# Performance work log

Measured on AMD Instinct MI355X. Metric: run time of the kernel, lower is better.

Reference implementation:

```python
import jax, jax.numpy as jnp
import numpy as np

# --- constants matching DILConfig ---
N_DIFF = 1000      # num_diffusion_steps
STEPS = 4          # inference_steps
S_MAX = 4          # max_scales
BUDGET = 0.2       # entropy_budget
G0 = 2.0           # guidance_strength
ENT_LO = 0.1       # stability_threshold_low
ENT_HI = 0.5       # stability_threshold_high
B, L, C, H = 16, 1024, 128, 512


def setup_inputs() -> dict:
    key = jax.random.key(0)
    ks = jax.random.split(key, 6)
    y_obs = jax.random.normal(ks[0], (B, L, C), dtype=jnp.float32)
    mask = (jax.random.uniform(ks[1], (B, L, C)) > 0.5).astype(jnp.float32)
    z_init = jax.random.normal(ks[2], (B, L, C), dtype=jnp.float32)
    W1 = jax.random.normal(ks[3], (C, H), dtype=jnp.float32) / np.sqrt(C)
    b1 = jnp.zeros((H,), dtype=jnp.float32)
    W2 = jax.random.normal(ks[4], (H, C), dtype=jnp.float32) / np.sqrt(H)
    b2 = jnp.zeros((C,), dtype=jnp.float32)
    tw = jax.random.normal(ks[5], (H,), dtype=jnp.float32)
    return {"y_obs": y_obs, "mask": mask, "z_init": z_init,
            "W1": W1, "b1": b1, "W2": W2, "b2": b2, "tw": tw}


def _dil_forward(y_obs, mask, z_init, W1, b1, W2, b2, tw):
    # diffusion schedule (linear betas)
    betas = jnp.linspace(1e-4, 0.02, N_DIFF, dtype=jnp.float32)
    ac = jnp.cumprod(1.0 - betas)
    alpha = jnp.sqrt(ac)                     # sqrt_alphas_cumprod
    sigma = jnp.sqrt(1.0 - ac)               # sqrt_one_minus_alphas_cumprod
    lam = jnp.log(alpha) - jnp.log(sigma)    # log-SNR/2

    step = N_DIFF // STEPS
    ks = [N_DIFF - 1 - i * step for i in range(STEPS)]

    def score(z, k):
        # epsilon predictor: channel MLP with scalar time feature
        t_feat = jnp.float32(k) / N_DIFF
        h = jax.nn.gelu(jnp.einsum('blc,ch->blh', z, W1) + b1 + t_feat * tw)
        return jnp.einsum('blh,hc->blc', h, W2) + b2

    z = z_init
    for k in ks:  # fixed small unrolled loop over inference steps
        kp = max(k - step, 0)
        eps = score(z, k)                                   # [B,L,C]
        h_lam = lam[kp] - lam[k]
        base_a = alpha[kp] / alpha[k]
        base_b = sigma[kp] * (jnp.exp(h_lam) - 1.0)

        # entropy map: batch-mean |eps| per pixel
        ent_pix = jnp.mean(jnp.abs(eps), axis=0)            # [L,C]

        # self-guidance on observed entries
        obs_err = (z - y_obs) * mask
        guidance = -obs_err / (jnp.var(obs_err) + 1e-8)     # [B,L,C]

        z_new = z
        # coarse -> fine so finer-scale selected nodes overwrite coarser ones
        for s in range(S_MAX - 1, -1, -1):
            w = 2 ** s
            pooled = ent_pix.reshape(L // w, w, C // w, w).mean(axis=(1, 3))
            Knodes = max(1, int(BUDGET * pooled.size))
            _, idx = jax.lax.top_k(pooled.ravel(), Knodes)
            selg = jnp.zeros((pooled.size,), jnp.float32).at[idx].set(1.0)
            selg = selg.reshape(pooled.shape)
            sel = jnp.repeat(jnp.repeat(selg, w, axis=0), w, axis=1)     # [L,C]
            ent_up = jnp.repeat(jnp.repeat(pooled, w, axis=0), w, axis=1)

            # adaptive solver order from entropy stability thresholds
            order = (1.0 + (ent_up > ENT_LO).astype(jnp.float32)
                         + (ent_up > ENT_HI).astype(jnp.float32))
            corr = (1.0 + (order - 1.0) * 0.5 * h_lam
                        + (order - 1.0) * (order - 2.0) / 6.0 * h_lam ** 2)
            gs = G0 * ent_up / (ent_up + 1.0)               # adaptive guidance

            cand = base_a * z - base_b * (corr * eps) + gs * guidance
            z_new = jnp.where(sel[None, :, :] > 0, cand, z_new)
        z = z_new
    return z


def reference(y_obs, mask, z_init, W1, b1, W2, b2, tw):
    return _dil_forward(y_obs, mask, z_init, W1, b1, W2, b2, tw)
```

## Files before the change

### kernel.cpp

```cpp
#include <hip/hip_runtime.h>
#include <math.h>
#include <stdint.h>

#define L_DIM 1024
#define C_DIM 128
#define H_DIM 512
#define B_DIM 16
#define LC (L_DIM * C_DIM)
#define BLC (B_DIM * LC)

typedef __attribute__((ext_vector_type(8))) short short8;
typedef __attribute__((ext_vector_type(4))) float floatx4;

__device__ __forceinline__ unsigned fordbits(unsigned u) {
    return (u & 0x80000000u) ? ~u : (u | 0x80000000u);
}

__device__ __forceinline__ void split3(float x, unsigned& uh, unsigned& um,
                                       unsigned& ul) {
    uh = __float_as_uint(x);
    const float r1 = x - __uint_as_float(uh & 0xffff0000u);
    um = __float_as_uint(r1);
    const float r2 = r1 - __uint_as_float(um & 0xffff0000u);
    ul = __float_as_uint(r2);
}

__device__ __forceinline__ float gelu_fast(float x) {
    const float g = 0.7978845608028654f * (x + 0.044715f * x * x * x);
    const float e = __expf(2.0f * g);
    const float t = 1.0f - 2.0f / (e + 1.0f);
    return 0.5f * x * (1.0f + t);
}

__global__ __launch_bounds__(256) void wsplit_kernel(
    const float* __restrict__ W1, const float* __restrict__ W2,
    unsigned short* __restrict__ W1h, unsigned short* __restrict__ W1m,
    unsigned short* __restrict__ W1l, unsigned short* __restrict__ W2h,
    unsigned short* __restrict__ W2m, unsigned short* __restrict__ W2l,
    unsigned* __restrict__ zeroblk) {
    const int t = blockIdx.x * 256 + threadIdx.x;
    if (t < 16396) zeroblk[t] = 0u;
    unsigned uh, um, ul;
    if (t < 65536) {
        const int j = t & 7, lane = (t >> 3) & 63, nt = (t >> 9) & 31,
                  kt = (t >> 14) & 3;
        const int k = kt * 32 + (lane >> 4) * 8 + j;
        const int n = nt * 16 + (lane & 15);
        split3(W1[k * 512 + n], uh, um, ul);
        W1h[t] = (unsigned short)(uh >> 16);
        W1m[t] = (unsigned short)(um >> 16);
        W1l[t] = (unsigned short)(ul >> 16);
    } else {
        const int t2 = t - 65536;
        const int j = t2 & 7, lane = (t2 >> 3) & 63, nt = (t2 >> 9) & 7,
                  kt = (t2 >> 12) & 15;
        const int k = kt * 32 + (lane >> 4) * 8 + j;
        const int n = nt * 16 + (lane & 15);
        split3(W2[k * 128 + n], uh, um, ul);
        W2h[t2] = (unsigned short)(uh >> 16);
        W2m[t2] = (unsigned short)(um >> 16);
        W2l[t2] = (unsigned short)(ul >> 16);
    }
}

#define MFMA6(AH, AM, AL, BH, BM, BL, ACC)                                    \
    ACC = __builtin_amdgcn_mfma_f32_16x16x32_bf16(AL, BH, ACC, 0, 0, 0);      \
    ACC = __builtin_amdgcn_mfma_f32_16x16x32_bf16(AM, BM, ACC, 0, 0, 0);      \
    ACC = __builtin_amdgcn_mfma_f32_16x16x32_bf16(AH, BL, ACC, 0, 0, 0);      \
    ACC = __builtin_amdgcn_mfma_f32_16x16x32_bf16(AM, BH, ACC, 0, 0, 0);      \
    ACC = __builtin_amdgcn_mfma_f32_16x16x32_bf16(AH, BM, ACC, 0, 0, 0);      \
    ACC = __builtin_amdgcn_mfma_f32_16x16x32_bf16(AH, BH, ACC, 0, 0, 0);

__device__ __forceinline__ int swz(int row, int col) {
    return row * 128 + ((((col >> 3) ^ (row & 15))) << 3) + (col & 7);
}

template <int UPD>
__global__ __launch_bounds__(1024, 8) void mlp_kernel(
    float* __restrict__ z, const float* __restrict__ zr,
    const float* __restrict__ y, const float* __restrict__ mk,
    const unsigned short* __restrict__ W1h, const unsigned short* __restrict__ W1m,
    const unsigned short* __restrict__ W1l, const unsigned short* __restrict__ W2h,
    const unsigned short* __restrict__ W2m, const unsigned short* __restrict__ W2l,
    const float* __restrict__ b1, const float* __restrict__ tw,
    const float* __restrict__ b2, float t_feat,
    float* __restrict__ eps_buf, float* __restrict__ ent,
    const float* __restrict__ cA, const float* __restrict__ cB,
    const float* __restrict__ cG, float* __restrict__ accum) {
    __shared__ unsigned short lds2[2][3][4096];
    __shared__ float red1[16], red2[16];
    const int tid = threadIdx.x;
    const int w = tid >> 6, lane = tid & 63;
    const int quad = lane >> 4, m16 = lane & 15;
    const int il_w = w >> 3, w8 = w & 7;
    const int l0 = blockIdx.x * 2;

    float s1 = 0.f, s2 = 0.f;
    {
        const int f = tid * 4;
        const int r_ = f >> 7, cb = f & 127;
        const int b = r_ & 15, il = r_ >> 4, l = l0 + il;
        const size_t g = ((size_t)b * 1024 + l) * 128 + cb;
        float4 zv = *(const float4*)(zr + g);
        const float4 yv = *(const float4*)(y + g);
        const float4 mv = *(const float4*)(mk + g);
        if (UPD) {
            const float4 ev = *(const float4*)(eps_buf + g);
            const int pix = l * 128 + cb;
            const float4 a4 = *(const float4*)(cA + pix);
            const float4 b4 = *(const float4*)(cB + pix);
            const float4 g4 = *(const float4*)(cG + pix);
            zv.x = a4.x * zv.x - b4.x * ev.x - g4.x * ((zv.x - yv.x) * mv.x);
            zv.y = a4.y * zv.y - b4.y * ev.y - g4.y * ((zv.y - yv.y) * mv.y);
            zv.z = a4.z * zv.z - b4.z * ev.z - g4.z * ((zv.z - yv.z) * mv.z);
            zv.w = a4.w * zv.w - b4.w * ev.w - g4.w * ((zv.w - yv.w) * mv.w);
            *(float4*)(z + g) = zv;
        }
        float oe;
        oe = (zv.x - yv.x) * mv.x; s1 += oe; s2 += oe * oe;
        oe = (zv.y - yv.y) * mv.y; s1 += oe; s2 += oe * oe;
        oe = (zv.z - yv.z) * mv.z; s1 += oe; s2 += oe * oe;
        oe = (zv.w - yv.w) * mv.w; s1 += oe; s2 += oe * oe;

        const int base = swz(r_, cb);
        const float xs[4] = {zv.x, zv.y, zv.z, zv.w};
        ushort4 vh, vm, vl;
        unsigned uh, um, ul;
        split3(xs[0], uh, um, ul); vh.x = uh >> 16; vm.x = um >> 16; vl.x = ul >> 16;
        split3(xs[1], uh, um, ul); vh.y = uh >> 16; vm.y = um >> 16; vl.y = ul >> 16;
        split3(xs[2], uh, um, ul); vh.z = uh >> 16; vm.z = um >> 16; vl.z = ul >> 16;
        split3(xs[3], uh, um, ul); vh.w = uh >> 16; vm.w = um >> 16; vl.w = ul >> 16;
        *(ushort4*)(&lds2[0][0][base]) = vh;
        *(ushort4*)(&lds2[0][1][base]) = vm;
        *(ushort4*)(&lds2[0][2][base]) = vl;
    }
#pragma unroll
    for (int off = 32; off; off >>= 1) {
        s1 += __shfl_down(s1, off);
        s2 += __shfl_down(s2, off);
    }
    if (lane == 0) { red1[w] = s1; red2[w] = s2; }
    __syncthreads();
    if (tid == 0) {
        float a1 = 0.f, a2 = 0.f;
#pragma unroll
        for (int i = 0; i < 16; ++i) { a1 += red1[i]; a2 += red2[i]; }
        atomicAdd(&accum[0], a1);
        atomicAdd(&accum[1], a2);
    }

    floatx4 acc1[4];
#pragma unroll
    for (int i = 0; i < 4; ++i) acc1[i] = (floatx4){0.f, 0.f, 0.f, 0.f};

#pragma unroll
    for (int kt = 0; kt < 4; ++kt) {
#pragma unroll
        for (int q2 = 0; q2 < 2; ++q2) {
            const size_t off = ((size_t)(kt * 32 + q2 * 16 + w) * 64 + lane) * 8;
            const short8 bh = *(const short8*)(W1h + off);
            const short8 bm = *(const short8*)(W1m + off);
            const short8 bl = *(const short8*)(W1l + off);
#pragma unroll
            for (int il = 0; il < 2; ++il) {
                const int fb = swz(il * 16 + m16, kt * 32 + quad * 8);
                const short8 Ah = *(const short8*)(&lds2[0][0][fb]);
                const short8 Am = *(const short8*)(&lds2[0][1][fb]);
                const short8 Al = *(const short8*)(&lds2[0][2][fb]);
                floatx4 a = acc1[q2 * 2 + il];
                MFMA6(Ah, Am, Al, bh, bm, bl, a);
                acc1[q2 * 2 + il] = a;
            }
        }
    }

    floatx4 acc2 = (floatx4){0.f, 0.f, 0.f, 0.f};

#pragma unroll
    for (int q = 0; q < 4; ++q) {
        const int bi = (q & 1) ^ 1;
        if (il_w == (q & 1)) {
            const int colg = q * 128 + w8 * 16 + m16;
            const float bb = b1[colg] + t_feat * tw[colg];
            const int kcol = w8 * 16 + m16;
#pragma unroll
            for (int il = 0; il < 2; ++il) {
#pragma unroll
                for (int r = 0; r < 4; ++r) {
                    const float x = gelu_fast(acc1[(q >> 1) * 2 + il][r] + bb);
                    unsigned uh, um, ul;
                    split3(x, uh, um, ul);
                    const int idx = swz(il * 16 + quad * 4 + r, kcol);
                    lds2[bi][0][idx] = (unsigned short)(uh >> 16);
                    lds2[bi][1][idx] = (unsigned short)(um >> 16);
                    lds2[bi][2][idx] = (unsigned short)(ul >> 16);
                }
            }
        }
        __syncthreads();

#pragma unroll
        for (int ktl = 0; ktl < 4; ++ktl) {
            const int fb = swz(il_w * 16 + m16, ktl * 32 + quad * 8);
            const short8 Ah2 = *(const short8*)(&lds2[bi][0][fb]);
            const short8 Am2 = *(const short8*)(&lds2[bi][1][fb]);
            const short8 Al2 = *(const short8*)(&lds2[bi][2][fb]);
            const size_t off =
                ((size_t)((q * 4 + ktl) * 8 + w8) * 64 + lane) * 8;
            const short8 bh = *(const short8*)(W2h + off);
            const short8 bm = *(const short8*)(W2m + off);
            const short8 bl = *(const short8*)(W2l + off);
            MFMA6(Ah2, Am2, Al2, bh, bm, bl, acc2);
        }
    }

    {
        const int col = w8 * 16 + m16;
        const float bb2 = b2[col];
        float pa = 0.f;
#pragma unroll
        for (int r = 0; r < 4; ++r) {
            const float e = acc2[r] + bb2;
            const int b = quad * 4 + r;
            eps_buf[((size_t)b * 1024 + l0 + il_w) * 128 + col] = e;
            pa += fabsf(e);
        }
        pa += __shfl_xor(pa, 16);
        pa += __shfl_xor(pa, 32);
        if (quad == 0) ent[(l0 + il_w) * 128 + col] = pa * (1.0f / 16.0f);
    }
}


__global__ __launch_bounds__(256) void pools_kernel(
    const float* __restrict__ ent, float* __restrict__ p1,
    float* __restrict__ p2, float* __restrict__ p3,
    unsigned* __restrict__ ghist) {
    __shared__ unsigned lh[8192];
    const int tid = threadIdx.x;
    const int gid = blockIdx.x * 256 + tid;
    for (int i = tid; i < 8192; i += 256) lh[i] = 0u;
    __syncthreads();

    {
        const float2 ev = *(const float2*)(ent + (size_t)gid * 2);
        const unsigned b0 = fordbits(__float_as_uint(ev.x)) >> 18;
        const unsigned b1_ = fordbits(__float_as_uint(ev.y)) >> 18;
        atomicAdd(&lh[b0 >> 1], 1u << ((b0 & 1) << 4));
        atomicAdd(&lh[b1_ >> 1], 1u << ((b1_ & 1) << 4));
    }
    if (gid < 32768) {
        const int r = gid >> 6, c = gid & 63;
        float s = 0.f;
#pragma unroll
        for (int ii = 0; ii < 2; ++ii) {
            const float2 e = *(const float2*)(ent + (((r * 2 + ii) << 7) + c * 2));
            s += e.x; s += e.y;
        }
        p1[gid] = s * 0.25f;
    }
    if (gid < 8192) {
        const int r = gid >> 5, c = gid & 31;
        float s = 0.f;
#pragma unroll
        for (int ii = 0; ii < 4; ++ii) {
            const float4 e = *(const float4*)(ent + (((r * 4 + ii) << 7) + c * 4));
            s += e.x; s += e.y; s += e.z; s += e.w;
        }
        p2[gid] = s * 0.0625f;
    }
    if (gid < 2048) {
        const int r = gid >> 4, c = gid & 15;
        float s = 0.f;
#pragma unroll
        for (int ii = 0; ii < 8; ++ii) {
            const float4 ea = *(const float4*)(ent + (((r * 8 + ii) << 7) + c * 8));
            const float4 eb = *(const float4*)(ent + (((r * 8 + ii) << 7) + c * 8 + 4));
            s += ea.x; s += ea.y; s += ea.z; s += ea.w;
            s += eb.x; s += eb.y; s += eb.z; s += eb.w;
        }
        p3[gid] = s * (1.0f / 64.0f);
    }
    __syncthreads();
    for (int i = tid; i < 8192; i += 256) {
        const unsigned v = lh[i];
        if (v & 0xFFFFu) atomicAdd(&ghist[2 * i], v & 0xFFFFu);
        if (v >> 16) atomicAdd(&ghist[2 * i + 1], v >> 16);
    }
}

#define CAND_CAP 16384

template <int NPT4, int N, unsigned K>
__device__ __forceinline__ void small_select(
    const float* __restrict__ data, unsigned* __restrict__ gout, const int t,
    const int w8, unsigned* __restrict__ histcand,
    unsigned* __restrict__ part, unsigned (*hrep)[512],
    unsigned* sh_b, unsigned* sh_krem, unsigned* sh_cnt, unsigned* sh_d,
    unsigned* sh_k2) {
    float4 xv[NPT4];
#pragma unroll
    for (int i = 0; i < NPT4; ++i) {
        const int idx4 = t + i * 1024;
        if (idx4 < (N >> 2)) xv[i] = ((const float4*)data)[idx4];
        else xv[i] = (float4){-1e30f, -1e30f, -1e30f, -1e30f};
    }
    unsigned u[NPT4 * 4];
#pragma unroll
    for (int i = 0; i < NPT4; ++i) {
        u[4 * i + 0] = fordbits(__float_as_uint(xv[i].x));
        u[4 * i + 1] = fordbits(__float_as_uint(xv[i].y));
        u[4 * i + 2] = fordbits(__float_as_uint(xv[i].z));
        u[4 * i + 3] = fordbits(__float_as_uint(xv[i].w));
    }
    if (t == 0) { *sh_b = 0u; *sh_krem = 1u; *sh_cnt = 0u; *sh_d = 0u; *sh_k2 = 1u; }
    for (int i = t; i < 16384; i += 1024) histcand[i] = 0u;
    __syncthreads();
#pragma unroll
    for (int j = 0; j < NPT4 * 4; ++j) atomicAdd(&histcand[u[j] >> 18], 1u);
    __syncthreads();
    {
        unsigned s = 0;
#pragma unroll
        for (int j = 0; j < 16; ++j) s += histcand[t * 16 + j];
        part[t] = s;
    }
    __syncthreads();
    for (int off = 1; off < 1024; off <<= 1) {
        const unsigned v = (t + off < 1024) ? part[t + off] : 0u;
        __syncthreads();
        part[t] += v;
        __syncthreads();
    }
    {
        const unsigned suf = part[t];
        const unsigned sufn = (t < 1023) ? part[t + 1] : 0u;
        if (suf >= K && sufn < K) {
            unsigned run = sufn;
            for (int b = 15; b >= 0; --b) {
                const unsigned hb = histcand[t * 16 + b];
                run += hb;
                if (run >= K) {
                    *sh_b = (unsigned)(t * 16 + b);
                    *sh_krem = K - (run - hb);
                    break;
                }
            }
        }
    }
    __syncthreads();
    const unsigned b14 = *sh_b;
    unsigned krem = *sh_krem;
    __syncthreads();
#pragma unroll
    for (int j = 0; j < NPT4 * 4; ++j)
        if ((u[j] >> 18) == b14) {
            const unsigned p = atomicAdd(sh_cnt, 1u);
            if (p < CAND_CAP) histcand[p] = u[j];
        }
    __syncthreads();
    const unsigned cnt = *sh_cnt;
    const bool inlds = (cnt <= CAND_CAP);
    for (int i = t; i < 4096; i += 1024) ((unsigned*)hrep)[i] = 0u;
    __syncthreads();
    if (inlds) {
        for (unsigned i = t; i < cnt; i += 1024)
            atomicAdd(&hrep[w8][(histcand[i] >> 9) & 511u], 1u);
    } else {
#pragma unroll
        for (int j = 0; j < NPT4 * 4; ++j)
            if ((u[j] >> 18) == b14)
                atomicAdd(&hrep[w8][(u[j] >> 9) & 511u], 1u);
    }
    __syncthreads();
    if (t < 512) {
        unsigned s = 0;
#pragma unroll
        for (int r = 0; r < 8; ++r) s += hrep[r][t];
        part[t] = s;
    }
    __syncthreads();
    for (int off = 1; off < 512; off <<= 1) {
        unsigned v = 0u;
        if (t < 512) v = (t + off < 512) ? part[t + off] : 0u;
        __syncthreads();
        if (t < 512) part[t] += v;
        __syncthreads();
    }
    if (t < 512) {
        const unsigned suf = part[t];
        const unsigned sufn = (t < 511) ? part[t + 1] : 0u;
        if (suf >= krem && sufn < krem) { *sh_d = (unsigned)t; *sh_k2 = krem - sufn; }
    }
    __syncthreads();
    const unsigned dA = *sh_d;
    krem = *sh_k2;
    __syncthreads();
    for (int i = t; i < 4096; i += 1024) ((unsigned*)hrep)[i] = 0u;
    __syncthreads();
    if (inlds) {
        for (unsigned i = t; i < cnt; i += 1024) {
            const unsigned c = histcand[i];
            if (((c >> 9) & 511u) == dA) atomicAdd(&hrep[w8][c & 511u], 1u);
        }
    } else {
#pragma unroll
        for (int j = 0; j < NPT4 * 4; ++j)
            if ((u[j] >> 18) == b14 && ((u[j] >> 9) & 511u) == dA)
                atomicAdd(&hrep[w8][u[j] & 511u], 1u);
    }
    __syncthreads();
    if (t < 512) {
        unsigned s = 0;
#pragma unroll
        for (int r = 0; r < 8; ++r) s += hrep[r][t];
        part[t] = s;
    }
    __syncthreads();
    for (int off = 1; off < 512; off <<= 1) {
        unsigned v = 0u;
        if (t < 512) v = (t + off < 512) ? part[t + off] : 0u;
        __syncthreads();
        if (t < 512) part[t] += v;
        __syncthreads();
    }
    if (t < 512) {
        const unsigned suf = part[t];
        const unsigned sufn = (t < 511) ? part[t + 1] : 0u;
        if (suf >= krem && sufn < krem)
            gout[0] = (b14 << 18) | (dA << 9) | (unsigned)t;
    }
}

__global__ __launch_bounds__(1024, 1) void thresh_kernel(
    const float* __restrict__ ent, const float* __restrict__ p1,
    const float* __restrict__ p2, const float* __restrict__ p3,
    const unsigned* __restrict__ ghist, unsigned* __restrict__ gprefix) {
    const int scale = blockIdx.x, t = threadIdx.x;
    __shared__ unsigned histcand[16384];
    __shared__ unsigned part[1024];
    __shared__ unsigned hrep[8][512];
    __shared__ unsigned sh_b, sh_krem, sh_cnt, sh_d, sh_k2;
    const int w8 = (t >> 6) & 7;

    if (scale == 1) {
        small_select<8, 32768, 6553u>(p1, &gprefix[1], t, w8, histcand, part,
                                      hrep, &sh_b, &sh_krem, &sh_cnt, &sh_d,
                                      &sh_k2);
        return;
    }
    if (scale == 2) {
        small_select<2, 8192, 1638u>(p2, &gprefix[2], t, w8, histcand, part,
                                     hrep, &sh_b, &sh_krem, &sh_cnt, &sh_d,
                                     &sh_k2);
        return;
    }
    if (scale == 3) {
        small_select<1, 2048, 409u>(p3, &gprefix[3], t, w8, histcand, part,
                                    hrep, &sh_b, &sh_krem, &sh_cnt, &sh_d,
                                    &sh_k2);
        return;
    }

    const unsigned K = 26214u;
    if (t == 0) { sh_b = 0u; sh_krem = 1u; sh_cnt = 0u; sh_d = 0u; sh_k2 = 1u; }

    {
        unsigned s = 0;
        const uint4* h4 = (const uint4*)(ghist + t * 16);
#pragma unroll
        for (int j = 0; j < 4; ++j) {
            const uint4 x = h4[j];
            s += x.x + x.y + x.z + x.w;
        }
        part[t] = s;
    }
    __syncthreads();
    for (int off = 1; off < 1024; off <<= 1) {
        const unsigned v = (t + off < 1024) ? part[t + off] : 0u;
        __syncthreads();
        part[t] += v;
        __syncthreads();
    }
    {
        const unsigned suf = part[t];
        const unsigned sufn = (t < 1023) ? part[t + 1] : 0u;
        if (suf >= K && sufn < K) {
            unsigned run = sufn;
            for (int b = 15; b >= 0; --b) {
                const unsigned hb = ghist[t * 16 + b];
                run += hb;
                if (run >= K) {
                    sh_b = (unsigned)(t * 16 + b);
                    sh_krem = K - (run - hb);
                    break;
                }
            }
        }
    }
    __syncthreads();
    const unsigned b14 = sh_b;
    unsigned krem = sh_krem;

    for (int base = 0; base < 32768; base += 8192) {
        float4 w4[8];
#pragma unroll
        for (int i = 0; i < 8; ++i)
            w4[i] = ((const float4*)ent)[base + i * 1024 + t];
#pragma unroll
        for (int i = 0; i < 8; ++i) {
            const float xs[4] = {w4[i].x, w4[i].y, w4[i].z, w4[i].w};
#pragma unroll
            for (int j = 0; j < 4; ++j) {
                const unsigned uu = fordbits(__float_as_uint(xs[j]));
                if ((uu >> 18) == b14) {
                    const unsigned p = atomicAdd(&sh_cnt, 1u);
                    if (p < CAND_CAP) histcand[p] = uu;
                }
            }
        }
    }
    __syncthreads();
    const unsigned cnt = sh_cnt;
    const bool inlds = (cnt <= CAND_CAP);

    for (int i = t; i < 4096; i += 1024) ((unsigned*)hrep)[i] = 0u;
    __syncthreads();
    if (inlds) {
        for (unsigned i = t; i < cnt; i += 1024)
            atomicAdd(&hrep[w8][(histcand[i] >> 9) & 511u], 1u);
    } else {
        for (int base = 0; base < 32768; base += 8192) {
            float4 w4[8];
#pragma unroll
            for (int i = 0; i < 8; ++i)
                w4[i] = ((const float4*)ent)[base + i * 1024 + t];
#pragma unroll
            for (int i = 0; i < 8; ++i) {
                const float xs[4] = {w4[i].x, w4[i].y, w4[i].z, w4[i].w};
#pragma unroll
                for (int j = 0; j < 4; ++j) {
                    const unsigned uu = fordbits(__float_as_uint(xs[j]));
                    if ((uu >> 18) == b14)
                        atomicAdd(&hrep[w8][(uu >> 9) & 511u], 1u);
                }
            }
        }
    }
    __syncthreads();
    if (t < 512) {
        unsigned s = 0;
#pragma unroll
        for (int r = 0; r < 8; ++r) s += hrep[r][t];
        part[t] = s;
    }
    __syncthreads();
    for (int off = 1; off < 512; off <<= 1) {
        unsigned v = 0u;
        if (t < 512) v = (t + off < 512) ? part[t + off] : 0u;
        __syncthreads();
        if (t < 512) part[t] += v;
        __syncthreads();
    }
    if (t < 512) {
        const unsigned suf = part[t];
        const unsigned sufn = (t < 511) ? part[t + 1] : 0u;
        if (suf >= krem && sufn < krem) { sh_d = (unsigned)t; sh_k2 = krem - sufn; }
    }
    __syncthreads();
    const unsigned dA = sh_d;
    krem = sh_k2;
    __syncthreads();

    for (int i = t; i < 4096; i += 1024) ((unsigned*)hrep)[i] = 0u;
    __syncthreads();
    if (inlds) {
        for (unsigned i = t; i < cnt; i += 1024) {
            const unsigned c = histcand[i];
            if (((c >> 9) & 511u) == dA) atomicAdd(&hrep[w8][c & 511u], 1u);
        }
    } else {
        for (int base = 0; base < 32768; base += 8192) {
            float4 w4[8];
#pragma unroll
            for (int i = 0; i < 8; ++i)
                w4[i] = ((const float4*)ent)[base + i * 1024 + t];
#pragma unroll
            for (int i = 0; i < 8; ++i) {
                const float xs[4] = {w4[i].x, w4[i].y, w4[i].z, w4[i].w};
#pragma unroll
                for (int j = 0; j < 4; ++j) {
                    const unsigned uu = fordbits(__float_as_uint(xs[j]));
                    if ((uu >> 18) == b14 && ((uu >> 9) & 511u) == dA)
                        atomicAdd(&hrep[w8][uu & 511u], 1u);
                }
            }
        }
    }
    __syncthreads();
    if (t < 512) {
        unsigned s = 0;
#pragma unroll
        for (int r = 0; r < 8; ++r) s += hrep[r][t];
        part[t] = s;
    }
    __syncthreads();
    for (int off = 1; off < 512; off <<= 1) {
        unsigned v = 0u;
        if (t < 512) v = (t + off < 512) ? part[t + off] : 0u;
        __syncthreads();
        if (t < 512) part[t] += v;
        __syncthreads();
    }
    if (t < 512) {
        const unsigned suf = part[t];
        const unsigned sufn = (t < 511) ? part[t + 1] : 0u;
        if (suf >= krem && sufn < krem)
            gprefix[0] = (b14 << 18) | (dA << 9) | (unsigned)t;
    }
}

__global__ __launch_bounds__(256) void coeff_kernel(
    const float* __restrict__ ent, const float* __restrict__ p1,
    const float* __restrict__ p2, const float* __restrict__ p3,
    const unsigned* __restrict__ gprefix, const float* __restrict__ accum_si,
    float* __restrict__ cA, float* __restrict__ cB, float* __restrict__ cG,
    unsigned* __restrict__ ghist, float base_a, float base_b, float h_lam) {
    const int i = blockIdx.x * 256 + threadIdx.x;
    if (i < 16384) ghist[i] = 0u;

    const unsigned t0 = gprefix[0], t1 = gprefix[1], t2 = gprefix[2],
                   t3 = gprefix[3];
    const float mean = accum_si[0] * (1.0f / (float)BLC);
    const float var = accum_si[1] * (1.0f / (float)BLC) - mean * mean;
    const float vinv = 1.0f / (var + 1e-8f);

    const int l = i >> 7, c = i & 127;
    float ent_v = 0.f;
    bool sel = false;
    const float v0 = ent[i];
    if (fordbits(__float_as_uint(v0)) >= t0) { ent_v = v0; sel = true; }
    else {
        const float v1 = p1[((l >> 1) << 6) + (c >> 1)];
        if (fordbits(__float_as_uint(v1)) >= t1) { ent_v = v1; sel = true; }
        else {
            const float v2 = p2[((l >> 2) << 5) + (c >> 2)];
            if (fordbits(__float_as_uint(v2)) >= t2) { ent_v = v2; sel = true; }
            else {
                const float v3 = p3[((l >> 3) << 4) + (c >> 3)];
                if (fordbits(__float_as_uint(v3)) >= t3) { ent_v = v3; sel = true; }
            }
        }
    }
    if (sel) {
        float corr;
        if (ent_v > 0.5f)
            corr = 1.0f + h_lam + h_lam * h_lam * (1.0f / 3.0f);
        else if (ent_v > 0.1f)
            corr = 1.0f + 0.5f * h_lam;
        else
            corr = 1.0f;
        cA[i] = base_a;
        cB[i] = base_b * corr;
        cG[i] = (2.0f * ent_v / (ent_v + 1.0f)) * vinv;
    } else {
        cA[i] = 1.0f;
        cB[i] = 0.f;
        cG[i] = 0.f;
    }
}

__global__ __launch_bounds__(256) void update_kernel(
    float* __restrict__ z, const float* __restrict__ y,
    const float* __restrict__ mk, const float* __restrict__ eps,
    const float* __restrict__ cA, const float* __restrict__ cB,
    const float* __restrict__ cG) {
    const int idx = blockIdx.x * 256 + threadIdx.x;
    const int p = idx & (LC - 1);
    const float zi = z[idx];
    z[idx] = cA[p] * zi - cB[p] * eps[idx] - cG[p] * ((zi - y[idx]) * mk[idx]);
}

extern "C" void kernel_launch(void* const* d_in, const int* in_sizes, int n_in,
                              void* d_out, int out_size, void* d_ws,
                              size_t ws_size, hipStream_t stream) {
    const float* y_obs = (const float*)d_in[0];
    const float* mask = (const float*)d_in[1];
    const float* z_init = (const float*)d_in[2];
    const float* W1 = (const float*)d_in[3];
    const float* b1 = (const float*)d_in[4];
    const float* W2 = (const float*)d_in[5];
    const float* b2 = (const float*)d_in[6];
    const float* tw = (const float*)d_in[7];
    float* z = (float*)d_out;
    float* ws = (float*)d_ws;

    float* eps = ws;
    float* ent = ws + 2097152;
    float* p1 = ws + 2228224;
    float* p2 = ws + 2260992;
    float* p3 = ws + 2269184;
    float* cA = ws + 2271232;
    float* cB = ws + 2402304;
    float* cG = ws + 2533376;
    float* accum = ws + 2664448;
    unsigned* gprefix = (unsigned*)(ws + 2664456);
    unsigned* ghist = (unsigned*)(ws + 2664460);
    unsigned short* W1h = (unsigned short*)(ws + 2680844);
    unsigned short* W1m = (unsigned short*)(ws + 2713612);
    unsigned short* W1l = (unsigned short*)(ws + 2746380);
    unsigned short* W2h = (unsigned short*)(ws + 2779148);
    unsigned short* W2m = (unsigned short*)(ws + 2811916);
    unsigned short* W2l = (unsigned short*)(ws + 2844684);

    float alpha_[1000], sigma_[1000], lam_[1000];
    {
        float ac = 1.0f;
        for (int i = 0; i < 1000; ++i) {
            const float beta = 1e-4f + (0.02f - 1e-4f) * ((float)i / 999.0f);
            ac = ac * (1.0f - beta);
            alpha_[i] = sqrtf(ac);
            sigma_[i] = sqrtf(1.0f - ac);
            lam_[i] = logf(alpha_[i]) - logf(sigma_[i]);
        }
    }
    float tf[4], hl[4], ba[4], bb[4];
    for (int si = 0; si < 4; ++si) {
        const int k = 999 - si * 250;
        const int kp = (k - 250 > 0) ? (k - 250) : 0;
        tf[si] = (float)k / 1000.0f;
        hl[si] = lam_[kp] - lam_[k];
        ba[si] = alpha_[kp] / alpha_[k];
        bb[si] = sigma_[kp] * (expf(hl[si]) - 1.0f);
    }

    wsplit_kernel<<<512, 256, 0, stream>>>(W1, W2, W1h, W1m, W1l, W2h, W2m,
                                           W2l, (unsigned*)accum);

    for (int si = 0; si < 4; ++si) {
        const float* zrd = (si <= 1) ? z_init : z;
        if (si == 0) {
            mlp_kernel<0><<<512, 1024, 0, stream>>>(
                z, zrd, y_obs, mask, W1h, W1m, W1l, W2h, W2m, W2l, b1, tw, b2,
                tf[0], eps, ent, cA, cB, cG, accum);
        } else {
            mlp_kernel<1><<<512, 1024, 0, stream>>>(
                z, zrd, y_obs, mask, W1h, W1m, W1l, W2h, W2m, W2l, b1, tw, b2,
                tf[si], eps, ent, cA, cB, cG, accum + 2 * si);
        }
        pools_kernel<<<256, 256, 0, stream>>>(ent, p1, p2, p3, ghist);
        thresh_kernel<<<4, 1024, 0, stream>>>(ent, p1, p2, p3, ghist, gprefix);
        coeff_kernel<<<512, 256, 0, stream>>>(ent, p1, p2, p3, gprefix,
                                              accum + 2 * si, cA, cB, cG,
                                              ghist, ba[si], bb[si], hl[si]);
    }
    update_kernel<<<8192, 256, 0, stream>>>(z, y_obs, mask, eps, cA, cB, cG);
}
```

Baseline: 415.9 us.

## Process four L rows per MLP block to reuse weight fragments across more tiles

Each MLP block now handles 64 rows (4 sequence positions × 16 batch) with 8 waves instead of 32 rows with 16 waves. Each wave loads a weight fragment once and applies it to 4 row tiles, halving global/L2 weight traffic per output. The double-buffered hidden LDS tile becomes a single buffer with an extra barrier per hidden chunk. Register pressure rises and the grid shrinks to 256 blocks, which reduces occupancy and latency hiding.

```diff
diff --git a/kernel.cpp b/kernel.cpp
--- a/kernel.cpp
+++ b/kernel.cpp
@@ -76,7 +76,7 @@
 }
 
 template <int UPD>
-__global__ __launch_bounds__(1024, 8) void mlp_kernel(
+__global__ __launch_bounds__(512, 2) void mlp_kernel(
     float* __restrict__ z, const float* __restrict__ zr,
     const float* __restrict__ y, const float* __restrict__ mk,
     const unsigned short* __restrict__ W1h, const unsigned short* __restrict__ W1m,
@@ -87,17 +87,18 @@
     float* __restrict__ eps_buf, float* __restrict__ ent,
     const float* __restrict__ cA, const float* __restrict__ cB,
     const float* __restrict__ cG, float* __restrict__ accum) {
-    __shared__ unsigned short lds2[2][3][4096];
-    __shared__ float red1[16], red2[16];
+    __shared__ unsigned short zA[3][8192];
+    __shared__ unsigned short hA[3][8192];
+    __shared__ float red1[8], red2[8];
     const int tid = threadIdx.x;
     const int w = tid >> 6, lane = tid & 63;
     const int quad = lane >> 4, m16 = lane & 15;
-    const int il_w = w >> 3, w8 = w & 7;
-    const int l0 = blockIdx.x * 2;
+    const int l0 = blockIdx.x * 4;
 
     float s1 = 0.f, s2 = 0.f;
-    {
-        const int f = tid * 4;
+#pragma unroll
+    for (int e = 0; e < 4; ++e) {
+        const int f = (e * 512 + tid) * 4;
         const int r_ = f >> 7, cb = f & 127;
         const int b = r_ & 15, il = r_ >> 4, l = l0 + il;
         const size_t g = ((size_t)b * 1024 + l) * 128 + cb;
@@ -130,9 +131,9 @@
         split3(xs[1], uh, um, ul); vh.y = uh >> 16; vm.y = um >> 16; vl.y = ul >> 16;
         split3(xs[2], uh, um, ul); vh.z = uh >> 16; vm.z = um >> 16; vl.z = ul >> 16;
         split3(xs[3], uh, um, ul); vh.w = uh >> 16; vm.w = um >> 16; vl.w = ul >> 16;
-        *(ushort4*)(&lds2[0][0][base]) = vh;
-        *(ushort4*)(&lds2[0][1][base]) = vm;
-        *(ushort4*)(&lds2[0][2][base]) = vl;
+        *(ushort4*)(&zA[0][base]) = vh;
+        *(ushort4*)(&zA[1][base]) = vm;
+        *(ushort4*)(&zA[2][base]) = vl;
     }
 #pragma unroll
     for (int off = 32; off; off >>= 1) {
@@ -144,56 +145,61 @@
     if (tid == 0) {
         float a1 = 0.f, a2 = 0.f;
 #pragma unroll
-        for (int i = 0; i < 16; ++i) { a1 += red1[i]; a2 += red2[i]; }
+        for (int i = 0; i < 8; ++i) { a1 += red1[i]; a2 += red2[i]; }
         atomicAdd(&accum[0], a1);
         atomicAdd(&accum[1], a2);
     }
 
-    floatx4 acc1[4];
-#pragma unroll
-    for (int i = 0; i < 4; ++i) acc1[i] = (floatx4){0.f, 0.f, 0.f, 0.f};
+    floatx4 acc1[16];
+#pragma unroll
+    for (int i = 0; i < 16; ++i) acc1[i] = (floatx4){0.f, 0.f, 0.f, 0.f};
 
 #pragma unroll
     for (int kt = 0; kt < 4; ++kt) {
-#pragma unroll
-        for (int q2 = 0; q2 < 2; ++q2) {
-            const size_t off = ((size_t)(kt * 32 + q2 * 16 + w) * 64 + lane) * 8;
+        short8 Ah[4], Am[4], Al[4];
+#pragma unroll
+        for (int il = 0; il < 4; ++il) {
+            const int fb = swz(il * 16 + m16, kt * 32 + quad * 8);
+            Ah[il] = *(const short8*)(&zA[0][fb]);
+            Am[il] = *(const short8*)(&zA[1][fb]);
+            Al[il] = *(const short8*)(&zA[2][fb]);
+        }
+#pragma unroll
+        for (int q = 0; q < 4; ++q) {
+            const size_t off = ((size_t)(kt * 32 + q * 8 + w) * 64 + lane) * 8;
             const short8 bh = *(const short8*)(W1h + off);
             const short8 bm = *(const short8*)(W1m + off);
             const short8 bl = *(const short8*)(W1l + off);
 #pragma unroll
-            for (int il = 0; il < 2; ++il) {
-                const int fb = swz(il * 16 + m16, kt * 32 + quad * 8);
-                const short8 Ah = *(const short8*)(&lds2[0][0][fb]);
-                const short8 Am = *(const short8*)(&lds2[0][1][fb]);
-                const short8 Al = *(const short8*)(&lds2[0][2][fb]);
-                floatx4 a = acc1[q2 * 2 + il];
-                MFMA6(Ah, Am, Al, bh, bm, bl, a);
-                acc1[q2 * 2 + il] = a;
-            }
-        }
-    }
-
-    floatx4 acc2 = (floatx4){0.f, 0.f, 0.f, 0.f};
+            for (int il = 0; il < 4; ++il) {
+                floatx4 a = acc1[q * 4 + il];
+                MFMA6(Ah[il], Am[il], Al[il], bh, bm, bl, a);
+                acc1[q * 4 + il] = a;
+            }
+        }
+    }
+
+    floatx4 acc2[4];
+#pragma unroll
+    for (int i = 0; i < 4; ++i) acc2[i] = (floatx4){0.f, 0.f, 0.f, 0.f};
 
 #pragma unroll
     for (int q = 0; q < 4; ++q) {
-        const int bi = (q & 1) ^ 1;
-        if (il_w == (q & 1)) {
-            const int colg = q * 128 + w8 * 16 + m16;
+        {
+            const int colg = q * 128 + w * 16 + m16;
             const float bb = b1[colg] + t_feat * tw[colg];
-            const int kcol = w8 * 16 + m16;
-#pragma unroll
-            for (int il = 0; il < 2; ++il) {
+            const int kcol = w * 16 + m16;
+#pragma unroll
+            for (int il = 0; il < 4; ++il) {
 #pragma unroll
                 for (int r = 0; r < 4; ++r) {
-                    const float x = gelu_fast(acc1[(q >> 1) * 2 + il][r] + bb);
+                    const float x = gelu_fast(acc1[q * 4 + il][r] + bb);
                     unsigned uh, um, ul;
                     split3(x, uh, um, ul);
                     const int idx = swz(il * 16 + quad * 4 + r, kcol);
-                    lds2[bi][0][idx] = (unsigned short)(uh >> 16);
-                    lds2[bi][1][idx] = (unsigned short)(um >> 16);
-                    lds2[bi][2][idx] = (unsigned short)(ul >> 16);
+                    hA[0][idx] = (unsigned short)(uh >> 16);
+                    hA[1][idx] = (unsigned short)(um >> 16);
+                    hA[2][idx] = (unsigned short)(ul >> 16);
                 }
             }
         }
@@ -201,33 +207,46 @@
 
 #pragma unroll
         for (int ktl = 0; ktl < 4; ++ktl) {
-            const int fb = swz(il_w * 16 + m16, ktl * 32 + quad * 8);
-            const short8 Ah2 = *(const short8*)(&lds2[bi][0][fb]);
-            const short8 Am2 = *(const short8*)(&lds2[bi][1][fb]);
-            const short8 Al2 = *(const short8*)(&lds2[bi][2][fb]);
+            short8 Ah2[4], Am2[4], Al2[4];
+#pragma unroll
+            for (int il = 0; il < 4; ++il) {
+                const int fb = swz(il * 16 + m16, ktl * 32 + quad * 8);
+                Ah2[il] = *(const short8*)(&hA[0][fb]);
+                Am2[il] = *(const short8*)(&hA[1][fb]);
+                Al2[il] = *(const short8*)(&hA[2][fb]);
+            }
             const size_t off =
-                ((size_t)((q * 4 + ktl) * 8 + w8) * 64 + lane) * 8;
+                ((size_t)((q * 4 + ktl) * 8 + w) * 64 + lane) * 8;
             const short8 bh = *(const short8*)(W2h + off);
             const short8 bm = *(const short8*)(W2m + off);
             const short8 bl = *(const short8*)(W2l + off);
-            MFMA6(Ah2, Am2, Al2, bh, bm, bl, acc2);
-        }
+#pragma unroll
+            for (int il = 0; il < 4; ++il) {
+                floatx4 a = acc2[il];
+                MFMA6(Ah2[il], Am2[il], Al2[il], bh, bm, bl, a);
+                acc2[il] = a;
+            }
+        }
+        __syncthreads();
     }
 
     {
-        const int col = w8 * 16 + m16;
+        const int col = w * 16 + m16;
         const float bb2 = b2[col];
-        float pa = 0.f;
-#pragma unroll
-        for (int r = 0; r < 4; ++r) {
-            const float e = acc2[r] + bb2;
-            const int b = quad * 4 + r;
-            eps_buf[((size_t)b * 1024 + l0 + il_w) * 128 + col] = e;
-            pa += fabsf(e);
-        }
-        pa += __shfl_xor(pa, 16);
-        pa += __shfl_xor(pa, 32);
-        if (quad == 0) ent[(l0 + il_w) * 128 + col] = pa * (1.0f / 16.0f);
+#pragma unroll
+        for (int il = 0; il < 4; ++il) {
+            float pa = 0.f;
+#pragma unroll
+            for (int r = 0; r < 4; ++r) {
+                const float e = acc2[il][r] + bb2;
+                const int b = quad * 4 + r;
+                eps_buf[((size_t)b * 1024 + l0 + il) * 128 + col] = e;
+                pa += fabsf(e);
+            }
+            pa += __shfl_xor(pa, 16);
+            pa += __shfl_xor(pa, 32);
+            if (quad == 0) ent[(l0 + il) * 128 + col] = pa * (1.0f / 16.0f);
+        }
     }
 }
 
@@ -740,11 +759,11 @@
     for (int si = 0; si < 4; ++si) {
         const float* zrd = (si <= 1) ? z_init : z;
         if (si == 0) {
-            mlp_kernel<0><<<512, 1024, 0, stream>>>(
+            mlp_kernel<0><<<256, 512, 0, stream>>>(
                 z, zrd, y_obs, mask, W1h, W1m, W1l, W2h, W2m, W2l, b1, tw, b2,
                 tf[0], eps, ent, cA, cB, cG, accum);
         } else {
-            mlp_kernel<1><<<512, 1024, 0, stream>>>(
+            mlp_kernel<1><<<256, 512, 0, stream>>>(
                 z, zrd, y_obs, mask, W1h, W1m, W1l, W2h, W2m, W2l, b1, tw, b2,
                 tf[si], eps, ent, cA, cB, cG, accum + 2 * si);
         }
```

Result: faster. 384.2 us (-7.6%).
